# Kernel tuning notes

Hardware: AMD Instinct MI355X
Metric: run time of the kernel (lower is better)

## Reference

```python
import jax, jax.numpy as jnp
import numpy as np

N_NODES = 50000
N_EDGES = 800000
IN_C, HID_C, OUT_C = 100, 128, 40


def setup_inputs() -> dict:
    key = jax.random.key(0)
    ks = jax.random.split(key, 10)
    x = jax.random.normal(ks[0], (N_NODES, IN_C), dtype=jnp.float32)
    edge_index = jax.random.randint(ks[1], (2, N_EDGES), 0, N_NODES, dtype=jnp.int64)

    def lin(k, fan_in, fan_out):
        kw, kb = jax.random.split(k)
        bound = 1.0 / np.sqrt(fan_in)
        W = jax.random.uniform(kw, (fan_in, fan_out), minval=-bound, maxval=bound, dtype=jnp.float32)
        b = jax.random.uniform(kb, (fan_out,), minval=-bound, maxval=bound, dtype=jnp.float32)
        return W, b

    W1a, b1a = lin(ks[2], IN_C, HID_C)
    W1b, b1b = lin(ks[3], HID_C, HID_C)
    W2a, b2a = lin(ks[4], HID_C, OUT_C)
    W2b, b2b = lin(ks[5], OUT_C, OUT_C)
    return {"x": x, "edge_index": edge_index,
            "W1a": W1a, "b1a": b1a, "W1b": W1b, "b1b": b1b,
            "W2a": W2a, "b2a": b2a, "W2b": W2b, "b2b": b2b}


def _gin_aggregate(x, src, dst):
    # GINConv with eps=0: (1+eps)*x_i + sum_{j in N(i)} x_j
    msg_sum = jax.ops.segment_sum(x[src], dst, num_segments=N_NODES)
    return x + msg_sum


def reference(x, edge_index, W1a, b1a, W1b, b1b, W2a, b2a, W2b, b2b):
    src, dst = edge_index[0], edge_index[1]
    # ---- layer 1: GINConv(MLP[in, hid, hid]) + ReLU (dropout is identity in eval)
    h = _gin_aggregate(x, src, dst)                      # [N, in]
    h = jax.nn.relu(h @ W1a + b1a) @ W1b + b1b           # [N, hid]
    h = jax.nn.relu(h)
    # ---- layer 2: GINConv(MLP[hid, out, out]), no trailing act
    h = _gin_aggregate(h, src, dst)                      # [N, hid]
    logits = jax.nn.relu(h @ W2a + b2a) @ W2b + b2b      # [N, out]
    return jax.nn.log_softmax(logits, axis=1)
```

## Files before the change

kernel.cpp:

```cpp
#include <hip/hip_runtime.h>

#define NNODES 50000
#define INC 100
#define HIDC 128
#define OUTC 40
#define NB2 50
#define BSZ2 1000
#define CAP2 24000
#define BIN_BLOCKS 256

typedef short bf16x8 __attribute__((ext_vector_type(8)));
typedef float f32x4 __attribute__((ext_vector_type(4)));

__device__ __forceinline__ unsigned short f2bf(float f) {
    unsigned int u = __float_as_uint(f);
    unsigned int r = (u + 0x7FFFu + ((u >> 16) & 1u)) >> 16;
    return (unsigned short)r;
}
__device__ __forceinline__ unsigned int pack2(float a, float b) {
    return (unsigned int)f2bf(a) | ((unsigned int)f2bf(b) << 16);
}
__device__ __forceinline__ float4 bf4(uint2 a) {
    return make_float4(__uint_as_float(a.x << 16), __uint_as_float(a.x & 0xFFFF0000u),
                       __uint_as_float(a.y << 16), __uint_as_float(a.y & 0xFFFF0000u));
}

__global__ __launch_bounds__(256) void prep_all(const float2* __restrict__ x2,
                                                unsigned int* __restrict__ xh, int n2,
                                                const float* __restrict__ W1a,
                                                unsigned short* __restrict__ Wt1a,
                                                const float* __restrict__ W1b,
                                                unsigned short* __restrict__ Wt1b,
                                                const float* __restrict__ W2a,
                                                unsigned short* __restrict__ Wt2a,
                                                const float* __restrict__ W2b,
                                                unsigned short* __restrict__ Wt2b) {
    int i = blockIdx.x * 256 + threadIdx.x;
    if (i < n2) {
        float2 v = x2[i];
        xh[i] = pack2(v.x, v.y);
        return;
    }
    i -= n2;
    if (i < 128 * 128) {
        int j = i >> 7, k = i & 127;
        Wt1a[i] = f2bf((k < INC) ? W1a[k * HIDC + j] : 0.f);
        return;
    }
    i -= 128 * 128;
    if (i < 128 * 128) {
        int j = i >> 7, k = i & 127;
        Wt1b[i] = f2bf(W1b[k * HIDC + j]);
        return;
    }
    i -= 128 * 128;
    if (i < 48 * 128) {
        int j = i >> 7, k = i & 127;
        Wt2a[i] = f2bf((j < OUTC) ? W2a[k * OUTC + j] : 0.f);
        return;
    }
    i -= 48 * 128;
    if (i < 48 * 64) {
        int j = i >> 6, k = i & 63;
        Wt2b[i] = f2bf((j < OUTC && k < OUTC) ? W2b[k * OUTC + j] : 0.f);
        return;
    }
}

__global__ __launch_bounds__(256) void bin_pairs(const int* __restrict__ src,
                                                 const int* __restrict__ dst,
                                                 int* __restrict__ bcnt,
                                                 unsigned int* __restrict__ pairs, int E) {
    __shared__ int bcount[NB2];
    __shared__ int bbase[NB2];
    __shared__ int bpos[NB2];
    int t = threadIdx.x;
    if (t < NB2) bcount[t] = 0;
    __syncthreads();
    int lo = (int)((long long)E * blockIdx.x / BIN_BLOCKS);
    int hi = (int)((long long)E * (blockIdx.x + 1) / BIN_BLOCKS);
    for (int e = lo + t; e < hi; e += 256) {
        int d = dst[e];
        atomicAdd(&bcount[d / BSZ2], 1);
    }
    __syncthreads();
    if (t < NB2) {
        bbase[t] = atomicAdd(&bcnt[t], bcount[t]);
        bpos[t] = 0;
    }
    __syncthreads();
    for (int e = lo + t; e < hi; e += 256) {
        int d = dst[e];
        int s = src[e];
        int b = d / BSZ2;
        int rk = atomicAdd(&bpos[b], 1);
        pairs[(size_t)b * CAP2 + bbase[b] + rk] = ((unsigned int)d << 16) | (unsigned int)s;
    }
}

__global__ __launch_bounds__(1024) void build_bucket(const unsigned int* __restrict__ pairs,
                                                     const int* __restrict__ bcnt,
                                                     int* __restrict__ offs,
                                                     unsigned short* __restrict__ csr) {
    __shared__ int hist[BSZ2];
    __shared__ int cur[BSZ2];
    __shared__ int wsum[16];
    __shared__ unsigned short lcsr[CAP2];
    __shared__ int base_s;

    const int b = blockIdx.x;
    const int t = threadIdx.x;

    if (t == 0) {
        int s = 0;
        for (int j = 0; j < b; ++j) s += bcnt[j];
        base_s = s;
    }
    for (int i = t; i < BSZ2; i += 1024) hist[i] = 0;
    __syncthreads();

    const int cnt = bcnt[b];
    const unsigned int* P = pairs + (size_t)b * CAP2;
    const int nlo = b * BSZ2;

    for (int i = t; i < cnt; i += 1024)
        atomicAdd(&hist[(int)(P[i] >> 16) - nlo], 1);
    __syncthreads();

    {
        int v = (t < BSZ2) ? hist[t] : 0;
        int lane = t & 63, wv = t >> 6;
        int incl = v;
#pragma unroll
        for (int off = 1; off < 64; off <<= 1) {
            int u = __shfl_up(incl, off);
            if (lane >= off) incl += u;
        }
        if (lane == 63) wsum[wv] = incl;
        __syncthreads();
        if (t == 0) {
            int s = 0;
#pragma unroll
            for (int j = 0; j < 16; ++j) { int x = wsum[j]; wsum[j] = s; s += x; }
        }
        __syncthreads();
        int excl = incl - v + wsum[wv];
        if (t < BSZ2) {
            cur[t] = excl;
            offs[nlo + t] = base_s + excl;
        }
        if (b == NB2 - 1 && t == 0) offs[NNODES] = base_s + cnt;
    }
    __syncthreads();

    for (int i = t; i < cnt; i += 1024) {
        unsigned int pr = P[i];
        int ln = (int)(pr >> 16) - nlo;
        int pos = atomicAdd(&cur[ln], 1);
        lcsr[pos] = (unsigned short)(pr & 0xFFFFu);
    }
    __syncthreads();

    for (int i = t; i < cnt; i += 1024) csr[base_s + i] = lcsr[i];
}

__global__ __launch_bounds__(256) void agg_wide_bf(const float4* __restrict__ self,
                                                   const uint2* __restrict__ featbf,
                                                   const int* __restrict__ offs,
                                                   const unsigned short* __restrict__ csr,
                                                   unsigned short* __restrict__ Abf, int N) {
    constexpr int C4 = 25;
    int node = blockIdx.x * 8 + (threadIdx.x >> 5);
    int l = threadIdx.x & 31;
    if (node >= N) return;
    if (l >= C4) {
        *reinterpret_cast<uint2*>(&Abf[(size_t)node * 128 + l * 4]) = make_uint2(0u, 0u);
        return;
    }
    int s = offs[node], e = offs[node + 1];
    float4 acc = self[(size_t)node * C4 + l];
    int i = s;
    for (; i + 8 <= e; i += 8) {
        int n0 = (int)csr[i + 0];
        int n1 = (int)csr[i + 1];
        int n2 = (int)csr[i + 2];
        int n3 = (int)csr[i + 3];
        int n4 = (int)csr[i + 4];
        int n5 = (int)csr[i + 5];
        int n6 = (int)csr[i + 6];
        int n7 = (int)csr[i + 7];
        float4 v0 = bf4(featbf[(size_t)n0 * C4 + l]);
        float4 v1 = bf4(featbf[(size_t)n1 * C4 + l]);
        float4 v2 = bf4(featbf[(size_t)n2 * C4 + l]);
        float4 v3 = bf4(featbf[(size_t)n3 * C4 + l]);
        float4 v4 = bf4(featbf[(size_t)n4 * C4 + l]);
        float4 v5 = bf4(featbf[(size_t)n5 * C4 + l]);
        float4 v6 = bf4(featbf[(size_t)n6 * C4 + l]);
        float4 v7 = bf4(featbf[(size_t)n7 * C4 + l]);
        acc.x += ((v0.x + v1.x) + (v2.x + v3.x)) + ((v4.x + v5.x) + (v6.x + v7.x));
        acc.y += ((v0.y + v1.y) + (v2.y + v3.y)) + ((v4.y + v5.y) + (v6.y + v7.y));
        acc.z += ((v0.z + v1.z) + (v2.z + v3.z)) + ((v4.z + v5.z) + (v6.z + v7.z));
        acc.w += ((v0.w + v1.w) + (v2.w + v3.w)) + ((v4.w + v5.w) + (v6.w + v7.w));
    }
    for (; i + 4 <= e; i += 4) {
        int n0 = (int)csr[i + 0];
        int n1 = (int)csr[i + 1];
        int n2 = (int)csr[i + 2];
        int n3 = (int)csr[i + 3];
        float4 v0 = bf4(featbf[(size_t)n0 * C4 + l]);
        float4 v1 = bf4(featbf[(size_t)n1 * C4 + l]);
        float4 v2 = bf4(featbf[(size_t)n2 * C4 + l]);
        float4 v3 = bf4(featbf[(size_t)n3 * C4 + l]);
        acc.x += (v0.x + v1.x) + (v2.x + v3.x);
        acc.y += (v0.y + v1.y) + (v2.y + v3.y);
        acc.z += (v0.z + v1.z) + (v2.z + v3.z);
        acc.w += (v0.w + v1.w) + (v2.w + v3.w);
    }
    for (; i < e; ++i) {
        int sn = (int)csr[i];
        float4 v = bf4(featbf[(size_t)sn * C4 + l]);
        acc.x += v.x; acc.y += v.y; acc.z += v.z; acc.w += v.w;
    }
    *reinterpret_cast<uint2*>(&Abf[(size_t)node * 128 + l * 4]) =
        make_uint2(pack2(acc.x, acc.y), pack2(acc.z, acc.w));
}

__global__ __launch_bounds__(256) void gemm_mfma128(const unsigned short* __restrict__ Abf,
                                                    const unsigned short* __restrict__ Wt,
                                                    const float* __restrict__ bias,
                                                    unsigned short* __restrict__ out, int N) {
    constexpr int LDW = 136;
    __shared__ unsigned short As[64 * LDW];
    __shared__ unsigned short Ws[128 * LDW];
    __shared__ float bs[128];

    const int tid = threadIdx.x;
    const int n0 = blockIdx.x * 64;

#pragma unroll
    for (int i = 0; i < 4; ++i) {
        int idx = tid + i * 256;
        int row = idx >> 4, c = idx & 15;
        int n = n0 + row;
        uint4 v = make_uint4(0u, 0u, 0u, 0u);
        if (n < N) v = *reinterpret_cast<const uint4*>(&Abf[(size_t)n * 128 + c * 8]);
        *reinterpret_cast<uint4*>(&As[row * LDW + c * 8]) = v;
    }
#pragma unroll
    for (int i = 0; i < 8; ++i) {
        int idx = tid + i * 256;
        int row = idx >> 4, c = idx & 15;
        uint4 v = *reinterpret_cast<const uint4*>(&Wt[(size_t)row * 128 + c * 8]);
        *reinterpret_cast<uint4*>(&Ws[row * LDW + c * 8]) = v;
    }
    if (tid < 128) bs[tid] = bias[tid];
    __syncthreads();

    const int w = tid >> 6, l = tid & 63;
    const int wr = w >> 1, wc = w & 1;
    const int r = l & 15, g = l >> 4;

    f32x4 acc[2][4];
#pragma unroll
    for (int rt = 0; rt < 2; ++rt)
#pragma unroll
        for (int ct = 0; ct < 4; ++ct) {
            float b = bs[wc * 64 + ct * 16 + r];
            acc[rt][ct] = (f32x4){b, b, b, b};
        }

#pragma unroll
    for (int s = 0; s < 4; ++s) {
        bf16x8 af[2], bfr[4];
#pragma unroll
        for (int rt = 0; rt < 2; ++rt)
            af[rt] = *reinterpret_cast<const bf16x8*>(
                &As[(wr * 32 + rt * 16 + r) * LDW + s * 32 + g * 8]);
#pragma unroll
        for (int ct = 0; ct < 4; ++ct)
            bfr[ct] = *reinterpret_cast<const bf16x8*>(
                &Ws[(wc * 64 + ct * 16 + r) * LDW + s * 32 + g * 8]);
#pragma unroll
        for (int rt = 0; rt < 2; ++rt)
#pragma unroll
            for (int ct = 0; ct < 4; ++ct)
                acc[rt][ct] = __builtin_amdgcn_mfma_f32_16x16x32_bf16(
                    af[rt], bfr[ct], acc[rt][ct], 0, 0, 0);
    }

#pragma unroll
    for (int rt = 0; rt < 2; ++rt) {
#pragma unroll
        for (int reg = 0; reg < 4; ++reg) {
            int n = n0 + wr * 32 + rt * 16 + 4 * g + reg;
            if (n < N) {
#pragma unroll
                for (int ct = 0; ct < 4; ++ct) {
                    int j = wc * 64 + ct * 16 + r;
                    float v = fmaxf(acc[rt][ct][reg], 0.f);
                    out[(size_t)n * 128 + j] = f2bf(v);
                }
            }
        }
    }
}

__global__ __launch_bounds__(256) void gemm_t2_mfma(const unsigned short* __restrict__ Abf,
                                                    const unsigned short* __restrict__ Wt,
                                                    unsigned short* __restrict__ Tb, int N) {
    constexpr int LDW = 136;
    __shared__ unsigned short As[64 * LDW];
    __shared__ unsigned short Ws[48 * LDW];

    const int tid = threadIdx.x;
    const int n0 = blockIdx.x * 64;

#pragma unroll
    for (int i = 0; i < 4; ++i) {
        int idx = tid + i * 256;
        int row = idx >> 4, c = idx & 15;
        int n = n0 + row;
        uint4 v = make_uint4(0u, 0u, 0u, 0u);
        if (n < N) v = *reinterpret_cast<const uint4*>(&Abf[(size_t)n * 128 + c * 8]);
        *reinterpret_cast<uint4*>(&As[row * LDW + c * 8]) = v;
    }
#pragma unroll
    for (int i = 0; i < 3; ++i) {
        int idx = tid + i * 256;
        int row = idx >> 4, c = idx & 15;
        uint4 v = *reinterpret_cast<const uint4*>(&Wt[(size_t)row * 128 + c * 8]);
        *reinterpret_cast<uint4*>(&Ws[row * LDW + c * 8]) = v;
    }
    __syncthreads();

    const int w = tid >> 6, l = tid & 63;
    const int r = l & 15, g = l >> 4;

    f32x4 acc[3] = {(f32x4){0,0,0,0}, (f32x4){0,0,0,0}, (f32x4){0,0,0,0}};

#pragma unroll
    for (int s = 0; s < 4; ++s) {
        bf16x8 af = *reinterpret_cast<const bf16x8*>(
            &As[(w * 16 + r) * LDW + s * 32 + g * 8]);
        bf16x8 bfr[3];
#pragma unroll
        for (int ct = 0; ct < 3; ++ct)
            bfr[ct] = *reinterpret_cast<const bf16x8*>(
                &Ws[(ct * 16 + r) * LDW + s * 32 + g * 8]);
#pragma unroll
        for (int ct = 0; ct < 3; ++ct)
            acc[ct] = __builtin_amdgcn_mfma_f32_16x16x32_bf16(af, bfr[ct], acc[ct], 0, 0, 0);
    }

#pragma unroll
    for (int reg = 0; reg < 4; ++reg) {
        int n = n0 + w * 16 + 4 * g + reg;
        if (n < N) {
#pragma unroll
            for (int ct = 0; ct < 3; ++ct) {
                int j = ct * 16 + r;
                if (j < OUTC) Tb[(size_t)n * OUTC + j] = f2bf(acc[ct][reg]);
            }
        }
    }
}

__global__ __launch_bounds__(256) void agg40_bf(const uint2* __restrict__ Tbf,
                                                const int* __restrict__ offs,
                                                const unsigned short* __restrict__ csr,
                                                float4* __restrict__ U, int N) {
    int wave = threadIdx.x >> 6;
    int lane = threadIdx.x & 63;
    int g = lane / 10;
    int sub = lane - g * 10;
    int node = blockIdx.x * 24 + wave * 6 + g;
    if (g >= 6 || node >= N) return;
    int s = offs[node], e = offs[node + 1];
    float4 acc = bf4(Tbf[(size_t)node * 10 + sub]);
    int i = s;
    for (; i + 8 <= e; i += 8) {
        int n0 = (int)csr[i + 0];
        int n1 = (int)csr[i + 1];
        int n2 = (int)csr[i + 2];
        int n3 = (int)csr[i + 3];
        int n4 = (int)csr[i + 4];
        int n5 = (int)csr[i + 5];
        int n6 = (int)csr[i + 6];
        int n7 = (int)csr[i + 7];
        float4 v0 = bf4(Tbf[(size_t)n0 * 10 + sub]);
        float4 v1 = bf4(Tbf[(size_t)n1 * 10 + sub]);
        float4 v2 = bf4(Tbf[(size_t)n2 * 10 + sub]);
        float4 v3 = bf4(Tbf[(size_t)n3 * 10 + sub]);
        float4 v4 = bf4(Tbf[(size_t)n4 * 10 + sub]);
        float4 v5 = bf4(Tbf[(size_t)n5 * 10 + sub]);
        float4 v6 = bf4(Tbf[(size_t)n6 * 10 + sub]);
        float4 v7 = bf4(Tbf[(size_t)n7 * 10 + sub]);
        acc.x += ((v0.x + v1.x) + (v2.x + v3.x)) + ((v4.x + v5.x) + (v6.x + v7.x));
        acc.y += ((v0.y + v1.y) + (v2.y + v3.y)) + ((v4.y + v5.y) + (v6.y + v7.y));
        acc.z += ((v0.z + v1.z) + (v2.z + v3.z)) + ((v4.z + v5.z) + (v6.z + v7.z));
        acc.w += ((v0.w + v1.w) + (v2.w + v3.w)) + ((v4.w + v5.w) + (v6.w + v7.w));
    }
    for (; i + 4 <= e; i += 4) {
        int n0 = (int)csr[i + 0];
        int n1 = (int)csr[i + 1];
        int n2 = (int)csr[i + 2];
        int n3 = (int)csr[i + 3];
        float4 v0 = bf4(Tbf[(size_t)n0 * 10 + sub]);
        float4 v1 = bf4(Tbf[(size_t)n1 * 10 + sub]);
        float4 v2 = bf4(Tbf[(size_t)n2 * 10 + sub]);
        float4 v3 = bf4(Tbf[(size_t)n3 * 10 + sub]);
        acc.x += (v0.x + v1.x) + (v2.x + v3.x);
        acc.y += (v0.y + v1.y) + (v2.y + v3.y);
        acc.z += (v0.z + v1.z) + (v2.z + v3.z);
        acc.w += (v0.w + v1.w) + (v2.w + v3.w);
    }
    for (; i < e; ++i) {
        int sn = (int)csr[i];
        float4 v = bf4(Tbf[(size_t)sn * 10 + sub]);
        acc.x += v.x; acc.y += v.y; acc.z += v.z; acc.w += v.w;
    }
    U[(size_t)node * 10 + sub] = acc;
}

__global__ __launch_bounds__(256) void epi40_mfma(const float* __restrict__ U,
                                                  const float* __restrict__ b2a,
                                                  const unsigned short* __restrict__ Wt2b,
                                                  const float* __restrict__ b2b,
                                                  float* __restrict__ out, int N) {
    constexpr int LDW = 72;
    __shared__ unsigned short As[64 * LDW];
    __shared__ unsigned short Ws[48 * LDW];
    __shared__ float ba[40], bb[40];

    const int tid = threadIdx.x;
    const int n0 = blockIdx.x * 64;

    if (tid < 40) { ba[tid] = b2a[tid]; bb[tid] = b2b[tid]; }
    for (int idx = tid; idx < 384; idx += 256) {
        int row = idx >> 3, c = idx & 7;
        uint4 v = *reinterpret_cast<const uint4*>(&Wt2b[row * 64 + c * 8]);
        *reinterpret_cast<uint4*>(&Ws[row * LDW + c * 8]) = v;
    }
    __syncthreads();

    for (int idx = tid; idx < 64 * 8; idx += 256) {
        int row = idx >> 3, c8 = idx & 7;
        int n = n0 + row;
        uint4 o = make_uint4(0u, 0u, 0u, 0u);
        if (c8 < 5 && n < N) {
            int j = c8 * 8;
            float4 u0 = *reinterpret_cast<const float4*>(&U[(size_t)n * 40 + j]);
            float4 u1 = *reinterpret_cast<const float4*>(&U[(size_t)n * 40 + j + 4]);
            float t0 = fmaxf(u0.x + ba[j + 0], 0.f);
            float t1 = fmaxf(u0.y + ba[j + 1], 0.f);
            float t2 = fmaxf(u0.z + ba[j + 2], 0.f);
            float t3 = fmaxf(u0.w + ba[j + 3], 0.f);
            float t4 = fmaxf(u1.x + ba[j + 4], 0.f);
            float t5 = fmaxf(u1.y + ba[j + 5], 0.f);
            float t6 = fmaxf(u1.z + ba[j + 6], 0.f);
            float t7 = fmaxf(u1.w + ba[j + 7], 0.f);
            o = make_uint4(pack2(t0, t1), pack2(t2, t3), pack2(t4, t5), pack2(t6, t7));
        }
        *reinterpret_cast<uint4*>(&As[row * LDW + c8 * 8]) = o;
    }
    __syncthreads();

    const int w = tid >> 6, l = tid & 63;
    const int r = l & 15, g = l >> 4;

    f32x4 acc[3] = {(f32x4){0,0,0,0}, (f32x4){0,0,0,0}, (f32x4){0,0,0,0}};
#pragma unroll
    for (int s = 0; s < 2; ++s) {
        bf16x8 af = *reinterpret_cast<const bf16x8*>(
            &As[(w * 16 + r) * LDW + s * 32 + g * 8]);
#pragma unroll
        for (int ct = 0; ct < 3; ++ct) {
            bf16x8 bfr = *reinterpret_cast<const bf16x8*>(
                &Ws[(ct * 16 + r) * LDW + s * 32 + g * 8]);
            acc[ct] = __builtin_amdgcn_mfma_f32_16x16x32_bf16(af, bfr, acc[ct], 0, 0, 0);
        }
    }

    float bb0 = bb[r], bb1 = bb[16 + r], bb2 = (r < 8) ? bb[32 + r] : 0.f;
#pragma unroll
    for (int reg = 0; reg < 4; ++reg) {
        int n = n0 + w * 16 + 4 * g + reg;
        float lg0 = acc[0][reg] + bb0;
        float lg1 = acc[1][reg] + bb1;
        float lg2 = (r < 8) ? acc[2][reg] + bb2 : -INFINITY;
        float m = fmaxf(fmaxf(lg0, lg1), lg2);
#pragma unroll
        for (int off = 1; off < 16; off <<= 1) m = fmaxf(m, __shfl_xor(m, off));
        float s = expf(lg0 - m) + expf(lg1 - m) + ((r < 8) ? expf(lg2 - m) : 0.f);
#pragma unroll
        for (int off = 1; off < 16; off <<= 1) s += __shfl_xor(s, off);
        float lse = m + logf(s);
        if (n < N) {
            out[(size_t)n * OUTC + r] = lg0 - lse;
            out[(size_t)n * OUTC + 16 + r] = lg1 - lse;
            if (r < 8) out[(size_t)n * OUTC + 32 + r] = lg2 - lse;
        }
    }
}

extern "C" void kernel_launch(void* const* d_in, const int* in_sizes, int n_in,
                              void* d_out, int out_size, void* d_ws, size_t ws_size,
                              hipStream_t stream) {
    const float* x   = (const float*)d_in[0];
    const int* edges = (const int*)d_in[1];
    const float* W1a = (const float*)d_in[2];
    const float* b1a = (const float*)d_in[3];
    const float* W1b = (const float*)d_in[4];
    const float* b1b = (const float*)d_in[5];
    const float* W2a = (const float*)d_in[6];
    const float* b2a = (const float*)d_in[7];
    const float* W2b = (const float*)d_in[8];
    const float* b2b = (const float*)d_in[9];

    const int N = NNODES;
    const int E = in_sizes[1] / 2;
    const int* srcp = edges;
    const int* dstp = edges + E;

    auto au = [](size_t v) { return (v + 255) & ~(size_t)255; };
    char* p = (char*)d_ws;
    int* bcnt    = (int*)p; p += au((size_t)NB2 * 4);
    int* offs    = (int*)p; p += au((size_t)(N + 1) * 4);
    unsigned int*   pairs = (unsigned int*)p;  p += au((size_t)NB2 * CAP2 * 4);
    unsigned short* csr   = (unsigned short*)p; p += au((size_t)E * 2);
    unsigned int*   xh   = (unsigned int*)p;   p += au((size_t)N * INC * 2);
    unsigned short* Abf  = (unsigned short*)p; p += au((size_t)N * 128 * 2);
    unsigned short* X1bf = (unsigned short*)p; p += au((size_t)N * 128 * 2);
    unsigned short* H1bf = (unsigned short*)p; p += au((size_t)N * 128 * 2);
    unsigned short* Tb   = (unsigned short*)p; p += au((size_t)N * OUTC * 2);
    float*          bufU = (float*)p;          p += au((size_t)N * OUTC * 4);
    unsigned short* Wt1a = (unsigned short*)p; p += au((size_t)128 * 128 * 2);
    unsigned short* Wt1b = (unsigned short*)p; p += au((size_t)128 * 128 * 2);
    unsigned short* Wt2a = (unsigned short*)p; p += au((size_t)48 * 128 * 2);
    unsigned short* Wt2b = (unsigned short*)p; p += au((size_t)48 * 64 * 2);

    const int n2 = N * INC / 2;
    const int prep_total = n2 + 128 * 128 + 128 * 128 + 48 * 128 + 48 * 64;

    prep_all<<<(prep_total + 255) / 256, 256, 0, stream>>>(
        (const float2*)x, xh, n2, W1a, Wt1a, W1b, Wt1b, W2a, Wt2a, W2b, Wt2b);

    hipMemsetAsync(bcnt, 0, (size_t)NB2 * sizeof(int), stream);
    bin_pairs<<<BIN_BLOCKS, 256, 0, stream>>>(srcp, dstp, bcnt, pairs, E);
    build_bucket<<<NB2, 1024, 0, stream>>>(pairs, bcnt, offs, csr);

    agg_wide_bf<<<(N + 7) / 8, 256, 0, stream>>>((const float4*)x, (const uint2*)xh,
                                                 offs, csr, Abf, N);
    gemm_mfma128<<<(N + 63) / 64, 256, 0, stream>>>(Abf, Wt1a, b1a, X1bf, N);
    gemm_mfma128<<<(N + 63) / 64, 256, 0, stream>>>(X1bf, Wt1b, b1b, H1bf, N);

    gemm_t2_mfma<<<(N + 63) / 64, 256, 0, stream>>>(H1bf, Wt2a, Tb, N);
    agg40_bf<<<(N + 23) / 24, 256, 0, stream>>>((const uint2*)Tb, offs, csr,
                                                (float4*)bufU, N);
    epi40_mfma<<<(N + 63) / 64, 256, 0, stream>>>(bufU, b2a, Wt2b, b2b, (float*)d_out, N);
}
```

Before: 120.3 us.

## Fuse three MLP GEMMs into one kernel and rebalance CSR bucket build

Merges the two 128-wide GEMMs and the layer-2 projection GEMM into a single kernel. The intermediate activations now stay in shared memory instead of passing through two N x 128 bf16 global buffers, which removes two launches and their global round trips. Separately, CSR bucketing moves to 200 smaller buckets built by 256-thread blocks, using a parallel shuffle reduction for the bucket base instead of a serial loop. The memset of bucket counters is folded into the prep kernel. The risk is a longer serial chain inside each fused block, with extra syncs and weight reloads, and possibly lower occupancy.

```diff
diff --git a/kernel.cpp b/kernel.cpp
--- a/kernel.cpp
+++ b/kernel.cpp
@@ -4,9 +4,9 @@
 #define INC 100
 #define HIDC 128
 #define OUTC 40
-#define NB2 50
-#define BSZ2 1000
-#define CAP2 24000
+#define NB2 200
+#define BSZ2 250
+#define CAP2 6400
 #define BIN_BLOCKS 256
 
 typedef short bf16x8 __attribute__((ext_vector_type(8)));
@@ -34,7 +34,9 @@
                                                 const float* __restrict__ W2a,
                                                 unsigned short* __restrict__ Wt2a,
                                                 const float* __restrict__ W2b,
-                                                unsigned short* __restrict__ Wt2b) {
+                                                unsigned short* __restrict__ Wt2b,
+                                                int* __restrict__ bcnt) {
+    if (blockIdx.x == 0 && threadIdx.x < NB2) bcnt[threadIdx.x] = 0;
     int i = blockIdx.x * 256 + threadIdx.x;
     if (i < n2) {
         float2 v = x2[i];
@@ -98,38 +100,42 @@
     }
 }
 
-__global__ __launch_bounds__(1024) void build_bucket(const unsigned int* __restrict__ pairs,
-                                                     const int* __restrict__ bcnt,
-                                                     int* __restrict__ offs,
-                                                     unsigned short* __restrict__ csr) {
+__global__ __launch_bounds__(256) void build_bucket(const unsigned int* __restrict__ pairs,
+                                                    const int* __restrict__ bcnt,
+                                                    int* __restrict__ offs,
+                                                    unsigned short* __restrict__ csr) {
     __shared__ int hist[BSZ2];
     __shared__ int cur[BSZ2];
-    __shared__ int wsum[16];
+    __shared__ int wsum[4];
+    __shared__ int redbuf[4];
     __shared__ unsigned short lcsr[CAP2];
     __shared__ int base_s;
 
     const int b = blockIdx.x;
     const int t = threadIdx.x;
-
-    if (t == 0) {
-        int s = 0;
-        for (int j = 0; j < b; ++j) s += bcnt[j];
-        base_s = s;
-    }
-    for (int i = t; i < BSZ2; i += 1024) hist[i] = 0;
-    __syncthreads();
+    const int lane = t & 63, wv = t >> 6;
+
+    {
+        int v = (t < b) ? bcnt[t] : 0;
+#pragma unroll
+        for (int off = 32; off; off >>= 1) v += __shfl_xor(v, off);
+        if (lane == 0) redbuf[wv] = v;
+    }
+    if (t < BSZ2) hist[t] = 0;
+    __syncthreads();
+    if (t == 0) base_s = redbuf[0] + redbuf[1] + redbuf[2] + redbuf[3];
 
     const int cnt = bcnt[b];
     const unsigned int* P = pairs + (size_t)b * CAP2;
     const int nlo = b * BSZ2;
-
-    for (int i = t; i < cnt; i += 1024)
+    __syncthreads();
+
+    for (int i = t; i < cnt; i += 256)
         atomicAdd(&hist[(int)(P[i] >> 16) - nlo], 1);
     __syncthreads();
 
     {
         int v = (t < BSZ2) ? hist[t] : 0;
-        int lane = t & 63, wv = t >> 6;
         int incl = v;
 #pragma unroll
         for (int off = 1; off < 64; off <<= 1) {
@@ -138,13 +144,11 @@
         }
         if (lane == 63) wsum[wv] = incl;
         __syncthreads();
-        if (t == 0) {
-            int s = 0;
-#pragma unroll
-            for (int j = 0; j < 16; ++j) { int x = wsum[j]; wsum[j] = s; s += x; }
-        }
-        __syncthreads();
-        int excl = incl - v + wsum[wv];
+        int wbase = 0;
+#pragma unroll
+        for (int j = 0; j < 4; ++j)
+            if (j < wv) wbase += wsum[j];
+        int excl = wbase + incl - v;
         if (t < BSZ2) {
             cur[t] = excl;
             offs[nlo + t] = base_s + excl;
@@ -153,15 +157,14 @@
     }
     __syncthreads();
 
-    for (int i = t; i < cnt; i += 1024) {
+    for (int i = t; i < cnt; i += 256) {
         unsigned int pr = P[i];
-        int ln = (int)(pr >> 16) - nlo;
-        int pos = atomicAdd(&cur[ln], 1);
+        int pos = atomicAdd(&cur[(int)(pr >> 16) - nlo], 1);
         lcsr[pos] = (unsigned short)(pr & 0xFFFFu);
     }
     __syncthreads();
 
-    for (int i = t; i < cnt; i += 1024) csr[base_s + i] = lcsr[i];
+    for (int i = t; i < cnt; i += 256) csr[base_s + i] = lcsr[i];
 }
 
 __global__ __launch_bounds__(256) void agg_wide_bf(const float4* __restrict__ self,
@@ -225,14 +228,17 @@
         make_uint2(pack2(acc.x, acc.y), pack2(acc.z, acc.w));
 }
 
-__global__ __launch_bounds__(256) void gemm_mfma128(const unsigned short* __restrict__ Abf,
-                                                    const unsigned short* __restrict__ Wt,
-                                                    const float* __restrict__ bias,
-                                                    unsigned short* __restrict__ out, int N) {
+__global__ __launch_bounds__(256) void fused_mlp(const unsigned short* __restrict__ Abf,
+                                                 const unsigned short* __restrict__ Wt1a,
+                                                 const float* __restrict__ b1a,
+                                                 const unsigned short* __restrict__ Wt1b,
+                                                 const float* __restrict__ b1b,
+                                                 const unsigned short* __restrict__ Wt2a,
+                                                 unsigned short* __restrict__ Tb, int N) {
     constexpr int LDW = 136;
     __shared__ unsigned short As[64 * LDW];
     __shared__ unsigned short Ws[128 * LDW];
-    __shared__ float bs[128];
+    __shared__ float bs1[128], bs2[128];
 
     const int tid = threadIdx.x;
     const int n0 = blockIdx.x * 64;
@@ -250,10 +256,10 @@
     for (int i = 0; i < 8; ++i) {
         int idx = tid + i * 256;
         int row = idx >> 4, c = idx & 15;
-        uint4 v = *reinterpret_cast<const uint4*>(&Wt[(size_t)row * 128 + c * 8]);
-        *reinterpret_cast<uint4*>(&Ws[row * LDW + c * 8]) = v;
-    }
-    if (tid < 128) bs[tid] = bias[tid];
+        *reinterpret_cast<uint4*>(&Ws[row * LDW + c * 8]) =
+            *reinterpret_cast<const uint4*>(&Wt1a[(size_t)row * 128 + c * 8]);
+    }
+    if (tid < 128) { bs1[tid] = b1a[tid]; bs2[tid] = b1b[tid]; }
     __syncthreads();
 
     const int w = tid >> 6, l = tid & 63;
@@ -265,10 +271,9 @@
     for (int rt = 0; rt < 2; ++rt)
 #pragma unroll
         for (int ct = 0; ct < 4; ++ct) {
-            float b = bs[wc * 64 + ct * 16 + r];
+            float b = bs1[wc * 64 + ct * 16 + r];
             acc[rt][ct] = (f32x4){b, b, b, b};
         }
-
 #pragma unroll
     for (int s = 0; s < 4; ++s) {
         bf16x8 af[2], bfr[4];
@@ -287,71 +292,87 @@
                 acc[rt][ct] = __builtin_amdgcn_mfma_f32_16x16x32_bf16(
                     af[rt], bfr[ct], acc[rt][ct], 0, 0, 0);
     }
-
-#pragma unroll
-    for (int rt = 0; rt < 2; ++rt) {
+    __syncthreads();
+
+#pragma unroll
+    for (int rt = 0; rt < 2; ++rt)
 #pragma unroll
         for (int reg = 0; reg < 4; ++reg) {
-            int n = n0 + wr * 32 + rt * 16 + 4 * g + reg;
-            if (n < N) {
-#pragma unroll
-                for (int ct = 0; ct < 4; ++ct) {
-                    int j = wc * 64 + ct * 16 + r;
-                    float v = fmaxf(acc[rt][ct][reg], 0.f);
-                    out[(size_t)n * 128 + j] = f2bf(v);
-                }
+            int row = wr * 32 + rt * 16 + 4 * g + reg;
+#pragma unroll
+            for (int ct = 0; ct < 4; ++ct) {
+                int col = wc * 64 + ct * 16 + r;
+                As[row * LDW + col] = f2bf(fmaxf(acc[rt][ct][reg], 0.f));
             }
         }
-    }
-}
-
-__global__ __launch_bounds__(256) void gemm_t2_mfma(const unsigned short* __restrict__ Abf,
-                                                    const unsigned short* __restrict__ Wt,
-                                                    unsigned short* __restrict__ Tb, int N) {
-    constexpr int LDW = 136;
-    __shared__ unsigned short As[64 * LDW];
-    __shared__ unsigned short Ws[48 * LDW];
-
-    const int tid = threadIdx.x;
-    const int n0 = blockIdx.x * 64;
-
-#pragma unroll
-    for (int i = 0; i < 4; ++i) {
+#pragma unroll
+    for (int i = 0; i < 8; ++i) {
         int idx = tid + i * 256;
         int row = idx >> 4, c = idx & 15;
-        int n = n0 + row;
-        uint4 v = make_uint4(0u, 0u, 0u, 0u);
-        if (n < N) v = *reinterpret_cast<const uint4*>(&Abf[(size_t)n * 128 + c * 8]);
-        *reinterpret_cast<uint4*>(&As[row * LDW + c * 8]) = v;
-    }
+        *reinterpret_cast<uint4*>(&Ws[row * LDW + c * 8]) =
+            *reinterpret_cast<const uint4*>(&Wt1b[(size_t)row * 128 + c * 8]);
+    }
+    __syncthreads();
+
+#pragma unroll
+    for (int rt = 0; rt < 2; ++rt)
+#pragma unroll
+        for (int ct = 0; ct < 4; ++ct) {
+            float b = bs2[wc * 64 + ct * 16 + r];
+            acc[rt][ct] = (f32x4){b, b, b, b};
+        }
+#pragma unroll
+    for (int s = 0; s < 4; ++s) {
+        bf16x8 af[2], bfr[4];
+#pragma unroll
+        for (int rt = 0; rt < 2; ++rt)
+            af[rt] = *reinterpret_cast<const bf16x8*>(
+                &As[(wr * 32 + rt * 16 + r) * LDW + s * 32 + g * 8]);
+#pragma unroll
+        for (int ct = 0; ct < 4; ++ct)
+            bfr[ct] = *reinterpret_cast<const bf16x8*>(
+                &Ws[(wc * 64 + ct * 16 + r) * LDW + s * 32 + g * 8]);
+#pragma unroll
+        for (int rt = 0; rt < 2; ++rt)
+#pragma unroll
+            for (int ct = 0; ct < 4; ++ct)
+                acc[rt][ct] = __builtin_amdgcn_mfma_f32_16x16x32_bf16(
+                    af[rt], bfr[ct], acc[rt][ct], 0, 0, 0);
+    }
+    __syncthreads();
+
+#pragma unroll
+    for (int rt = 0; rt < 2; ++rt)
+#pragma unroll
+        for (int reg = 0; reg < 4; ++reg) {
+            int row = wr * 32 + rt * 16 + 4 * g + reg;
+#pragma unroll
+            for (int ct = 0; ct < 4; ++ct) {
+                int col = wc * 64 + ct * 16 + r;
+                As[row * LDW + col] = f2bf(fmaxf(acc[rt][ct][reg], 0.f));
+            }
+        }
 #pragma unroll
     for (int i = 0; i < 3; ++i) {
         int idx = tid + i * 256;
         int row = idx >> 4, c = idx & 15;
-        uint4 v = *reinterpret_cast<const uint4*>(&Wt[(size_t)row * 128 + c * 8]);
-        *reinterpret_cast<uint4*>(&Ws[row * LDW + c * 8]) = v;
-    }
-    __syncthreads();
-
-    const int w = tid >> 6, l = tid & 63;
-    const int r = l & 15, g = l >> 4;
-
-    f32x4 acc[3] = {(f32x4){0,0,0,0}, (f32x4){0,0,0,0}, (f32x4){0,0,0,0}};
-
+        *reinterpret_cast<uint4*>(&Ws[row * LDW + c * 8]) =
+            *reinterpret_cast<const uint4*>(&Wt2a[(size_t)row * 128 + c * 8]);
+    }
+    __syncthreads();
+
+    f32x4 acc3[3] = {(f32x4){0, 0, 0, 0}, (f32x4){0, 0, 0, 0}, (f32x4){0, 0, 0, 0}};
 #pragma unroll
     for (int s = 0; s < 4; ++s) {
         bf16x8 af = *reinterpret_cast<const bf16x8*>(
             &As[(w * 16 + r) * LDW + s * 32 + g * 8]);
-        bf16x8 bfr[3];
-#pragma unroll
-        for (int ct = 0; ct < 3; ++ct)
-            bfr[ct] = *reinterpret_cast<const bf16x8*>(
+#pragma unroll
+        for (int ct = 0; ct < 3; ++ct) {
+            bf16x8 bfr = *reinterpret_cast<const bf16x8*>(
                 &Ws[(ct * 16 + r) * LDW + s * 32 + g * 8]);
-#pragma unroll
-        for (int ct = 0; ct < 3; ++ct)
-            acc[ct] = __builtin_amdgcn_mfma_f32_16x16x32_bf16(af, bfr[ct], acc[ct], 0, 0, 0);
-    }
-
+            acc3[ct] = __builtin_amdgcn_mfma_f32_16x16x32_bf16(af, bfr, acc3[ct], 0, 0, 0);
+        }
+    }
 #pragma unroll
     for (int reg = 0; reg < 4; ++reg) {
         int n = n0 + w * 16 + 4 * g + reg;
@@ -359,7 +380,7 @@
 #pragma unroll
             for (int ct = 0; ct < 3; ++ct) {
                 int j = ct * 16 + r;
-                if (j < OUTC) Tb[(size_t)n * OUTC + j] = f2bf(acc[ct][reg]);
+                if (j < OUTC) Tb[(size_t)n * OUTC + j] = f2bf(acc3[ct][reg]);
             }
         }
     }
@@ -468,7 +489,7 @@
     const int w = tid >> 6, l = tid & 63;
     const int r = l & 15, g = l >> 4;
 
-    f32x4 acc[3] = {(f32x4){0,0,0,0}, (f32x4){0,0,0,0}, (f32x4){0,0,0,0}};
+    f32x4 acc[3] = {(f32x4){0, 0, 0, 0}, (f32x4){0, 0, 0, 0}, (f32x4){0, 0, 0, 0}};
 #pragma unroll
     for (int s = 0; s < 2; ++s) {
         bf16x8 af = *reinterpret_cast<const bf16x8*>(
@@ -530,8 +551,6 @@
     unsigned short* csr   = (unsigned short*)p; p += au((size_t)E * 2);
     unsigned int*   xh   = (unsigned int*)p;   p += au((size_t)N * INC * 2);
     unsigned short* Abf  = (unsigned short*)p; p += au((size_t)N * 128 * 2);
-    unsigned short* X1bf = (unsigned short*)p; p += au((size_t)N * 128 * 2);
-    unsigned short* H1bf = (unsigned short*)p; p += au((size_t)N * 128 * 2);
     unsigned short* Tb   = (unsigned short*)p; p += au((size_t)N * OUTC * 2);
     float*          bufU = (float*)p;          p += au((size_t)N * OUTC * 4);
     unsigned short* Wt1a = (unsigned short*)p; p += au((size_t)128 * 128 * 2);
@@ -543,18 +562,15 @@
     const int prep_total = n2 + 128 * 128 + 128 * 128 + 48 * 128 + 48 * 64;
 
     prep_all<<<(prep_total + 255) / 256, 256, 0, stream>>>(
-        (const float2*)x, xh, n2, W1a, Wt1a, W1b, Wt1b, W2a, Wt2a, W2b, Wt2b);
-
-    hipMemsetAsync(bcnt, 0, (size_t)NB2 * sizeof(int), stream);
+        (const float2*)x, xh, n2, W1a, Wt1a, W1b, Wt1b, W2a, Wt2a, W2b, Wt2b, bcnt);
+
     bin_pairs<<<BIN_BLOCKS, 256, 0, stream>>>(srcp, dstp, bcnt, pairs, E);
-    build_bucket<<<NB2, 1024, 0, stream>>>(pairs, bcnt, offs, csr);
+    build_bucket<<<NB2, 256, 0, stream>>>(pairs, bcnt, offs, csr);
 
     agg_wide_bf<<<(N + 7) / 8, 256, 0, stream>>>((const float4*)x, (const uint2*)xh,
                                                  offs, csr, Abf, N);
-    gemm_mfma128<<<(N + 63) / 64, 256, 0, stream>>>(Abf, Wt1a, b1a, X1bf, N);
-    gemm_mfma128<<<(N + 63) / 64, 256, 0, stream>>>(X1bf, Wt1b, b1b, H1bf, N);
-
-    gemm_t2_mfma<<<(N + 63) / 64, 256, 0, stream>>>(H1bf, Wt2a, Tb, N);
+    fused_mlp<<<(N + 63) / 64, 256, 0, stream>>>(Abf, Wt1a, b1a, Wt1b, b1b, Wt2a, Tb, N);
+
     agg40_bf<<<(N + 23) / 24, 256, 0, stream>>>((const uint2*)Tb, offs, csr,
                                                 (float4*)bufU, N);
     epi40_mfma<<<(N + 63) / 64, 256, 0, stream>>>(bufU, b2a, Wt2b, b2b, (float*)d_out, N);
```

After: 103.1 us. 14.3% less time.
